# Kernel tuning notes

Hardware: AMD Instinct MI355X
Metric: run time of the kernel (lower is better)

The kernel has to match this reference:

```python
import jax, jax.numpy as jnp
import numpy as np

N = 16384          # replayed items
D_STATE = 2048     # state_dim
D_SEM = 1024       # semantic_dim
S = 4096           # num_semantic_slots
LR = 0.01
DIST_THRESH = 2.0


def setup_inputs() -> dict:
    key = jax.random.key(0)
    k1, k2, k3 = jax.random.split(key, 3)
    replayed_states = jax.random.normal(k1, (N, D_STATE), dtype=jnp.float32)
    replayed_rewards = jax.random.normal(k2, (N,), dtype=jnp.float32)
    # small weight scale so projected content std ~0.05 -> nearest distances
    # straddle the 2.0 threshold and both branches get exercised
    W = jax.random.normal(k3, (D_SEM, D_STATE), dtype=jnp.float32) * (0.05 / np.sqrt(D_STATE))
    b = jnp.zeros((D_SEM,), dtype=jnp.float32)
    semantic_traces = jnp.zeros((S, D_SEM), dtype=jnp.float32)
    trace_strengths = jnp.zeros((S,), dtype=jnp.float32)
    return {
        "replayed_states": replayed_states,
        "replayed_rewards": replayed_rewards,
        "W": W,
        "b": b,
        "semantic_traces": semantic_traces,
        "trace_strengths": trace_strengths,
    }


def _consolidate(content_all, rewards, traces0, strengths0):
    slot_ids = jnp.arange(S, dtype=jnp.int32)

    def step(carry, xs):
        traces, strengths, ptr, num = carry
        content, reward = xs
        reward = jnp.abs(reward)
        valid = jnp.minimum(num, S)
        # euclidean distances to valid slots (invalid -> +inf)
        d = jnp.sqrt(jnp.sum((traces - content[None, :]) ** 2, axis=1))
        d = jnp.where(slot_ids < valid, d, jnp.inf)
        nearest = jnp.argmin(d).astype(jnp.int32)
        nearest_dist = d[nearest]
        do_update = (num > 0) & (nearest_dist < DIST_THRESH)

        # branch A: EMA update of nearest slot
        eff_lr = LR * (1.0 + reward)
        delta = content - traces[nearest]
        traces_u = traces.at[nearest].add(delta * eff_lr)
        strengths_u = strengths.at[nearest].add(1.0)

        # branch B: insert at ring-buffer ptr
        traces_i = traces.at[ptr].set(content)
        strengths_i = strengths.at[ptr].set(1.0)
        ptr_i = (ptr + 1) % S
        num_i = jnp.minimum(num + 1, S)

        traces_n = jnp.where(do_update, traces_u, traces_i)
        strengths_n = jnp.where(do_update, strengths_u, strengths_i)
        ptr_n = jnp.where(do_update, ptr, ptr_i)
        num_n = jnp.where(do_update, num, num_i)
        return (traces_n, strengths_n, ptr_n, num_n), None

    init = (traces0, strengths0, jnp.int32(0), jnp.int32(0))
    (traces, strengths, ptr, num), _ = jax.lax.scan(step, init, (content_all, rewards))
    return traces, strengths, num


def reference(replayed_states, replayed_rewards, W, b, semantic_traces, trace_strengths):
    # projection: nn.Linear -> x @ W.T + b
    content_all = replayed_states @ W.T + b  # (N, D_SEM)
    traces, strengths, num = _consolidate(
        content_all, replayed_rewards, semantic_traces, trace_strengths
    )
    valid_mask = (jnp.arange(S) < jnp.minimum(num, S)).astype(jnp.float32)
    denom = jnp.maximum(valid_mask.sum(), 1.0)
    mean_strength = jnp.where(num > 0, (strengths * valid_mask).sum() / denom, 0.0)
    num_consolidated = jnp.int32(N)  # every item either updates or inserts
    return traces, strengths, num, num_consolidated, mean_strength


if __name__ == "__main__":
    out = reference(**setup_inputs())
    print([getattr(o, "shape", o) for o in out])
```

## Files before the change

### kernel.cpp

```cpp
#include <hip/hip_runtime.h>
#include <cstdint>
#include <cstddef>

#define N_ITEMS 16384
#define D_STATE 2048
#define D_SEM   1024
#define S_SLOTS 4096
#define DTHRESH 2.0f

#define B_ITEMS 256
#define NBLK    (N_ITEMS / B_ITEMS)
#define CHUNK_BLKS 16
#define CHUNK_ITEMS (B_ITEMS * CHUNK_BLKS)

typedef unsigned long long u64;
typedef unsigned int u32;

__global__ __launch_bounds__(256)
void gemm_kernel(const float* __restrict__ A, const float* __restrict__ W,
                 const float* __restrict__ bias, float* __restrict__ C) {
  __shared__ float As[16][68];
  __shared__ float Bs[16][68];
  const int t = threadIdx.x;
  const int ty = t >> 4, tx = t & 15;
  const int i0 = blockIdx.x * 64, j0 = blockIdx.y * 64;
  const int lrow = t >> 2, lcol = (t & 3) << 2;
  float acc[4][4] = {{0.f}};
  const float* ap = A + (size_t)(i0 + lrow) * D_STATE + lcol;
  const float* wp = W + (size_t)(j0 + lrow) * D_STATE + lcol;
  for (int k0 = 0; k0 < D_STATE; k0 += 16) {
    float4 av = *(const float4*)(ap + k0);
    float4 wv = *(const float4*)(wp + k0);
    __syncthreads();
    As[lcol + 0][lrow] = av.x; As[lcol + 1][lrow] = av.y;
    As[lcol + 2][lrow] = av.z; As[lcol + 3][lrow] = av.w;
    Bs[lcol + 0][lrow] = wv.x; Bs[lcol + 1][lrow] = wv.y;
    Bs[lcol + 2][lrow] = wv.z; Bs[lcol + 3][lrow] = wv.w;
    __syncthreads();
#pragma unroll
    for (int kk = 0; kk < 16; kk++) {
      float a[4], b[4];
#pragma unroll
      for (int y = 0; y < 4; y++) a[y] = As[kk][ty * 4 + y];
#pragma unroll
      for (int x = 0; x < 4; x++) b[x] = Bs[kk][tx * 4 + x];
#pragma unroll
      for (int y = 0; y < 4; y++)
#pragma unroll
        for (int x = 0; x < 4; x++) acc[y][x] = fmaf(a[y], b[x], acc[y][x]);
    }
  }
#pragma unroll
  for (int y = 0; y < 4; y++)
#pragma unroll
    for (int x = 0; x < 4; x++) {
      const int col = j0 + tx * 4 + x;
      C[(size_t)(i0 + ty * 4 + y) * D_SEM + col] = acc[y][x] + bias[col];
    }
}

__global__ __launch_bounds__(256)
void gram_kernel(const float* __restrict__ Cc, float* __restrict__ G) {
  const int z = blockIdx.z;
  const float* A = Cc + (size_t)z * B_ITEMS * D_SEM;
  __shared__ float As[16][68];
  __shared__ float Bs[16][68];
  const int t = threadIdx.x;
  const int ty = t >> 4, tx = t & 15;
  const int i0 = blockIdx.x * 64, j0 = blockIdx.y * 64;
  const int lrow = t >> 2, lcol = (t & 3) << 2;
  float acc[4][4] = {{0.f}};
  const float* ap = A + (size_t)(i0 + lrow) * D_SEM + lcol;
  const float* wp = A + (size_t)(j0 + lrow) * D_SEM + lcol;
  for (int k0 = 0; k0 < D_SEM; k0 += 16) {
    float4 av = *(const float4*)(ap + k0);
    float4 wv = *(const float4*)(wp + k0);
    __syncthreads();
    As[lcol + 0][lrow] = av.x; As[lcol + 1][lrow] = av.y;
    As[lcol + 2][lrow] = av.z; As[lcol + 3][lrow] = av.w;
    Bs[lcol + 0][lrow] = wv.x; Bs[lcol + 1][lrow] = wv.y;
    Bs[lcol + 2][lrow] = wv.z; Bs[lcol + 3][lrow] = wv.w;
    __syncthreads();
#pragma unroll
    for (int kk = 0; kk < 16; kk++) {
      float a[4], b[4];
#pragma unroll
      for (int y = 0; y < 4; y++) a[y] = As[kk][ty * 4 + y];
#pragma unroll
      for (int x = 0; x < 4; x++) b[x] = Bs[kk][tx * 4 + x];
#pragma unroll
      for (int y = 0; y < 4; y++)
#pragma unroll
        for (int x = 0; x < 4; x++) acc[y][x] = fmaf(a[y], b[x], acc[y][x]);
    }
  }
  float* Gz = G + (size_t)z * B_ITEMS * B_ITEMS;
#pragma unroll
  for (int y = 0; y < 4; y++)
#pragma unroll
    for (int x = 0; x < 4; x++)
      Gz[(size_t)(i0 + ty * 4 + y) * B_ITEMS + j0 + tx * 4 + x] = acc[y][x];
}

__global__ __launch_bounds__(256)
void pgemm_kernel(const float* __restrict__ A,
                  const float* __restrict__ T,
                  float* __restrict__ P,
                  const int* __restrict__ state) {
  const int limit = min(state[0] + B_ITEMS, S_SLOTS);
  const int j0 = blockIdx.y * 64;
  const int i0 = blockIdx.x * 64;
  const int t = threadIdx.x;
  const int ty = t >> 4, tx = t & 15;
  if (j0 >= limit) {
    const float4 z = {0.f, 0.f, 0.f, 0.f};
    const int col = j0 + tx * 4;
#pragma unroll
    for (int y = 0; y < 4; y++)
      *(float4*)(P + (size_t)(i0 + ty * 4 + y) * S_SLOTS + col) = z;
    return;
  }
  __shared__ float As[16][68];
  __shared__ float Bs[16][68];
  const int lrow = t >> 2, lcol = (t & 3) << 2;
  float acc[4][4] = {{0.f}};
  const float* ap = A + (size_t)(i0 + lrow) * D_SEM + lcol;
  const float* wp = T + (size_t)(j0 + lrow) * D_SEM + lcol;
  for (int k0 = 0; k0 < D_SEM; k0 += 16) {
    float4 av = *(const float4*)(ap + k0);
    float4 wv = *(const float4*)(wp + k0);
    __syncthreads();
    As[lcol + 0][lrow] = av.x; As[lcol + 1][lrow] = av.y;
    As[lcol + 2][lrow] = av.z; As[lcol + 3][lrow] = av.w;
    Bs[lcol + 0][lrow] = wv.x; Bs[lcol + 1][lrow] = wv.y;
    Bs[lcol + 2][lrow] = wv.z; Bs[lcol + 3][lrow] = wv.w;
    __syncthreads();
#pragma unroll
    for (int kk = 0; kk < 16; kk++) {
      float a[4], b[4];
#pragma unroll
      for (int y = 0; y < 4; y++) a[y] = As[kk][ty * 4 + y];
#pragma unroll
      for (int x = 0; x < 4; x++) b[x] = Bs[kk][tx * 4 + x];
#pragma unroll
      for (int y = 0; y < 4; y++)
#pragma unroll
        for (int x = 0; x < 4; x++) acc[y][x] = fmaf(a[y], b[x], acc[y][x]);
    }
  }
#pragma unroll
  for (int y = 0; y < 4; y++)
#pragma unroll
    for (int x = 0; x < 4; x++)
      P[(size_t)(i0 + ty * 4 + y) * S_SLOTS + j0 + tx * 4 + x] = acc[y][x];
}

__global__ __launch_bounds__(256)
void init_kernel(const float* __restrict__ traces0, float* __restrict__ out,
                 float* __restrict__ n_g, int* __restrict__ state) {
  __shared__ float wsum[4];
  const int s = blockIdx.x, t = threadIdx.x;
  const int lane = t & 63, wave = t >> 6;
  float4 v = *(const float4*)(traces0 + (size_t)s * D_SEM + 4 * t);
  *(float4*)(out + (size_t)s * D_SEM + 4 * t) = v;
  float nn = v.x * v.x + v.y * v.y + v.z * v.z + v.w * v.w;
#pragma unroll
  for (int o = 32; o; o >>= 1) nn += __shfl_down(nn, o, 64);
  if (lane == 0) wsum[wave] = nn;
  __syncthreads();
  if (t == 0) n_g[s] = wsum[0] + wsum[1] + wsum[2] + wsum[3];
  if (s == 0 && t == 0) { state[0] = 0; state[1] = 0; }
}

__device__ __forceinline__ float wave_min_f32(float x) {
  int xi = __float_as_int(x), y;
  y = __builtin_amdgcn_update_dpp(xi, xi, 0x111, 0xF, 0xF, false);
  x = fminf(x, __int_as_float(y)); xi = __float_as_int(x);
  y = __builtin_amdgcn_update_dpp(xi, xi, 0x112, 0xF, 0xF, false);
  x = fminf(x, __int_as_float(y)); xi = __float_as_int(x);
  y = __builtin_amdgcn_update_dpp(xi, xi, 0x114, 0xF, 0xF, false);
  x = fminf(x, __int_as_float(y)); xi = __float_as_int(x);
  y = __builtin_amdgcn_update_dpp(xi, xi, 0x118, 0xF, 0xF, false);
  x = fminf(x, __int_as_float(y)); xi = __float_as_int(x);
  y = __builtin_amdgcn_update_dpp(xi, xi, 0x142, 0xA, 0xF, false);
  x = fminf(x, __int_as_float(y)); xi = __float_as_int(x);
  y = __builtin_amdgcn_update_dpp(xi, xi, 0x143, 0xC, 0xF, false);
  x = fminf(x, __int_as_float(y)); xi = __float_as_int(x);
  return __int_as_float(__builtin_amdgcn_readlane(xi, 63));
}

#define CORR_SZ 4352
#define SWZ(s) ((s) + ((s) >> 4))

__global__ __launch_bounds__(512, 1)
void scan_kernel(const float* __restrict__ P, const float* __restrict__ Gb,
                 const float* __restrict__ rewards, const float* __restrict__ n_g,
                 int* __restrict__ state, u64* __restrict__ decs) {
  __shared__ float corr0[CORR_SZ];
  __shared__ float corr1[CORR_SZ];
  __shared__ float grow[8][B_ITEMS];
  __shared__ float rew_l[B_ITEMS];
  __shared__ u64 partials[2][8];
  const int t = threadIdx.x;
  const int lane = t & 63, wave = t >> 6;
  const int s_base = t << 3;
  const int c_base = s_base + (t >> 1);

  int num = state[0];
  int ptr = state[1];

  for (int s = t; s < CORR_SZ; s += 512) { corr0[s] = 0.f; corr1[s] = 0.f; }
  if (t < B_ITEMS) {
    rew_l[t] = rewards[t];
    grow[0][t] = Gb[t];
    grow[1][t] = Gb[B_ITEMS + t];
  }
  float pend_a = (t < B_ITEMS) ? Gb[2 * B_ITEMS + t] : 0.f;
  float pend_b = (t < B_ITEMS) ? Gb[3 * B_ITEMS + t] : 0.f;

  float n_reg[8];
#pragma unroll
  for (int k = 0; k < 8; k += 4) {
    float4 nv = *(const float4*)(n_g + s_base + k);
    n_reg[k + 0] = (s_base + k + 0 < num) ? nv.x : __uint_as_float(0x7F800000u);
    n_reg[k + 1] = (s_base + k + 1 < num) ? nv.y : __uint_as_float(0x7F800000u);
    n_reg[k + 2] = (s_base + k + 2 < num) ? nv.z : __uint_as_float(0x7F800000u);
    n_reg[k + 3] = (s_base + k + 3 < num) ? nv.w : __uint_as_float(0x7F800000u);
  }
  float alpha_r[8];
#pragma unroll
  for (int k = 0; k < 8; k++) alpha_r[k] = 1.f;

  float p_cur[8];
#pragma unroll
  for (int k = 0; k < 8; k += 4) {
    float4 v0 = *(const float4*)(P + s_base + k);
    p_cur[k] = v0.x; p_cur[k + 1] = v0.y; p_cur[k + 2] = v0.z; p_cur[k + 3] = v0.w;
  }

  float raw_a[8], raw_b[8];
  {
    const float* rp = P + (size_t)S_SLOTS + s_base;
#pragma unroll
    for (int k = 0; k < 8; k += 4) {
      float4 v = *(const float4*)(rp + k);
      raw_a[k] = v.x; raw_a[k + 1] = v.y; raw_a[k + 2] = v.z; raw_a[k + 3] = v.w;
    }
#pragma unroll
    for (int k = 0; k < 8; k++) raw_b[k] = 0.f;
  }

  int my_cslot = -1; float my_coeff = 0.f;
  u32 my_slot = 0; float my_lr = 0.f;

  __syncthreads();

#define OWNFIX(K, I) { const float nold = n_reg[K]; \
    if (upd) { \
      n_reg[K] = omr * omr * nold + 2.0f * lr * omr * p_cur[K] + lr * lr * gi_l; \
      alpha_r[K] = __fmul_rn(alpha_r[K], omr); \
      if ((I) + 1 < B_ITEMS) cv[K] = fmaf(omr, cv[K], __fmul_rn(lr, g1)); \
    } else { n_reg[K] = gi_l; alpha_r[K] = 0.f; \
      if ((I) + 1 < B_ITEMS) cv[K] = g1; } }

#define SCAN_STEP(I, CBUF, RAWC, RAWN, PEND) { \
     \
    if (t < B_ITEMS) { \
      if ((I) + 2 < B_ITEMS) grow[((I) + 2) & 7][t] = PEND; \
      if ((I) + 4 < B_ITEMS) PEND = Gb[(size_t)((I) + 4) * B_ITEMS + t]; \
    } \
     \
    if ((I) + 2 < B_ITEMS) { \
      const float* rp = P + (size_t)((I) + 2) * S_SLOTS + s_base; \
      _Pragma("unroll") \
      for (int k = 0; k < 8; k += 4) { \
        float4 v = *(const float4*)(rp + k); \
        RAWN[k] = v.x; RAWN[k + 1] = v.y; RAWN[k + 2] = v.z; RAWN[k + 3] = v.w; \
      } \
    } \
     \
    const float gi_l = grow[(I) & 7][(I)]; \
    const float riv = rew_l[(I)]; \
    float g1 = 0.f; \
    if ((I) + 1 < B_ITEMS) g1 = grow[(I) & 7][(I) + 1]; \
     \
    if ((I) + 1 < B_ITEMS && my_coeff != 0.f) \
      atomicAdd(&CBUF[SWZ(my_cslot)], \
                __fmul_rn(my_coeff, grow[((I) + 1) & 7][t])); \
     \
    float d2[8]; \
    _Pragma("unroll") \
    for (int k = 0; k < 8; k++) { \
      const float v = fmaf(-2.0f, p_cur[k], n_reg[k] + gi_l); \
      d2[k] = (v > 0.f) ? v : 0.f; \
    } \
    float dloc = d2[0]; \
    _Pragma("unroll") \
    for (int k = 1; k < 8; k++) dloc = fminf(dloc, d2[k]); \
    u32 iloc = 0; \
    _Pragma("unroll") \
    for (int k = 7; k >= 1; k--) if (d2[k] == dloc) iloc = (u32)k; \
    const u32 sloc = (u32)s_base + iloc; \
     \
    const float dmin = wave_min_f32(dloc); \
    const u64 bmask = __ballot(dloc == dmin); \
    const int bl = __ffsll((unsigned long long)bmask) - 1; \
    const u32 swave = (u32)__builtin_amdgcn_readlane((int)sloc, bl); \
    if (lane == 0) \
      partials[(I) & 1][wave] = ((u64)__float_as_uint(dmin) << 32) | swave; \
    asm volatile("s_waitcnt lgkmcnt(0)" ::: "memory"); \
    __builtin_amdgcn_s_barrier(); \
    __builtin_amdgcn_sched_barrier(0); \
     \
    u64 bk = partials[(I) & 1][0]; \
    { u64 v = partials[(I) & 1][1]; if (v < bk) bk = v; \
      v = partials[(I) & 1][2]; if (v < bk) bk = v; \
      v = partials[(I) & 1][3]; if (v < bk) bk = v; \
      v = partials[(I) & 1][4]; if (v < bk) bk = v; \
      v = partials[(I) & 1][5]; if (v < bk) bk = v; \
      v = partials[(I) & 1][6]; if (v < bk) bk = v; \
      v = partials[(I) & 1][7]; if (v < bk) bk = v; } \
    float cv[8]; \
    if ((I) + 1 < B_ITEMS) { \
      _Pragma("unroll") \
      for (int k = 0; k < 8; k++) cv[k] = CBUF[c_base + k]; \
    } else { \
      _Pragma("unroll") \
      for (int k = 0; k < 8; k++) cv[k] = 0.f; \
    } \
    const float d2b = __uint_as_float((u32)(bk >> 32)); \
    const int nslot = (int)(u32)bk; \
    const bool upd = (num > 0) && (d2b < 4.0f); \
    const float lr = __fmul_rn(0.01f, __fadd_rn(1.0f, fabsf(riv))); \
    const int slot = upd ? nslot : ptr; \
    const float omr = 1.0f - lr; \
    if (!upd) { num = min(num + 1, S_SLOTS); ptr = (ptr + 1) & (S_SLOTS - 1); } \
    if ((I) == t) { my_slot = (u32)slot | (upd ? 0x80000000u : 0u); my_lr = lr; } \
    if (my_cslot == slot) my_coeff = upd ? __fmul_rn(my_coeff, omr) : 0.f; \
    if ((I) == t) { my_cslot = slot; my_coeff = upd ? lr : 1.f; } \
     \
    if ((slot >> 3) == t) { \
      switch (slot & 7) { \
        case 0:  OWNFIX(0, I) break; case 1:  OWNFIX(1, I) break; \
        case 2:  OWNFIX(2, I) break; case 3:  OWNFIX(3, I) break; \
        case 4:  OWNFIX(4, I) break; case 5:  OWNFIX(5, I) break; \
        case 6:  OWNFIX(6, I) break; default: OWNFIX(7, I) break; \
      } \
    } \
     \
    if ((I) + 1 < B_ITEMS) { \
      _Pragma("unroll") \
      for (int k = 0; k < 8; k++) { \
        p_cur[k] = fmaf(alpha_r[k], RAWC[k], cv[k]); \
        CBUF[c_base + k] = 0.f; \
      } \
    } \
  }

  for (int i = 0; i < B_ITEMS; i += 2) {
    SCAN_STEP(i,     corr0, raw_a, raw_b, pend_a)
    SCAN_STEP(i + 1, corr1, raw_b, raw_a, pend_b)
  }
#undef SCAN_STEP
#undef OWNFIX

  if (t == 0) { state[0] = num; state[1] = ptr; }
  if (t < B_ITEMS)
    decs[t] = ((u64)__float_as_uint(my_lr) << 32) | (u64)my_slot;
}

__global__ __launch_bounds__(256)
void apply_kernel(const float* __restrict__ content,
                  const u64* __restrict__ decs,
                  float* __restrict__ traces,
                  float* __restrict__ n_g) {
  __shared__ u32 aslot[B_ITEMS];
  __shared__ float alr[B_ITEMS];
  __shared__ float betas[B_ITEMS];
  __shared__ int notowner;
  __shared__ float wsum[4];
  const int t = threadIdx.x, j = blockIdx.x;
  const int lane = t & 63, wave = t >> 6;
  const u64 d = decs[t];
  aslot[t] = (u32)(d & 0xFFFFFFFFull);
  alr[t] = __uint_as_float((u32)(d >> 32));
  if (t == 0) notowner = 0;
  __syncthreads();
  const u32 myslot = aslot[j] & 0x7FFFFFFFu;
  if (t > j && (aslot[t] & 0x7FFFFFFFu) == myslot) notowner = 1;
  __syncthreads();
  if (notowner) return;

  float alpha = 1.f, beta = 0.f;
  for (int k = 0; k < B_ITEMS; k++) {
    const u32 a = aslot[k];
    if ((a & 0x7FFFFFFFu) == myslot) {
      const float lr = alr[k];
      if (a & 0x80000000u) {
        const float om = 1.f - lr;
        alpha *= om; beta *= om;
        if (t == k) beta += lr;
      } else {
        alpha = 0.f; beta = (t == k) ? 1.f : 0.f;
      }
    }
  }
  betas[t] = beta;
  __syncthreads();

  float4 v = *(const float4*)(traces + (size_t)myslot * D_SEM + 4 * t);
  v.x *= alpha; v.y *= alpha; v.z *= alpha; v.w *= alpha;
  for (int k = 0; k < B_ITEMS; k++) {
    if ((aslot[k] & 0x7FFFFFFFu) == myslot) {
      const float bk = betas[k];
      const float4 c = *(const float4*)(content + (size_t)k * D_SEM + 4 * t);
      v.x = fmaf(bk, c.x, v.x); v.y = fmaf(bk, c.y, v.y);
      v.z = fmaf(bk, c.z, v.z); v.w = fmaf(bk, c.w, v.w);
    }
  }
  *(float4*)(traces + (size_t)myslot * D_SEM + 4 * t) = v;
  float nn = v.x * v.x + v.y * v.y + v.z * v.z + v.w * v.w;
#pragma unroll
  for (int o = 32; o; o >>= 1) nn += __shfl_down(nn, o, 64);
  if (lane == 0) wsum[wave] = nn;
  __syncthreads();
  if (t == 0) n_g[myslot] = wsum[0] + wsum[1] + wsum[2] + wsum[3];
}

__global__ __launch_bounds__(256)
void finalize_kernel(const float* __restrict__ strengths0,
                     const u64* __restrict__ decs,
                     const int* __restrict__ state, float* __restrict__ out) {
  __shared__ int last_ins[S_SLOTS];
  __shared__ int cnt[S_SLOTS];
  __shared__ float wsum[4];
  const int t = threadIdx.x, lane = t & 63, wave = t >> 6;
  for (int s = t; s < S_SLOTS; s += 256) { last_ins[s] = -1; cnt[s] = 0; }
  __syncthreads();
  for (int k = t; k < N_ITEMS; k += 256) {
    const u32 dd = (u32)(decs[k] & 0xFFFFFFFFull);
    if (!(dd & 0x80000000u)) atomicMax(&last_ins[(int)dd], k);
  }
  __syncthreads();
  for (int k = t; k < N_ITEMS; k += 256) {
    const u32 dd = (u32)(decs[k] & 0xFFFFFFFFull);
    const int slot = (int)(dd & 0x7FFFFFFFu);
    if ((dd & 0x80000000u) && k > last_ins[slot]) atomicAdd(&cnt[slot], 1);
  }
  __syncthreads();
  const int num = state[0];
  float* outs = out + (size_t)S_SLOTS * D_SEM;
  float lsum = 0.f;
  for (int s = t; s < S_SLOTS; s += 256) {
    const float base = (last_ins[s] >= 0) ? 1.f : strengths0[s];
    const float v = base + (float)cnt[s];
    outs[s] = v;
    if (s < num) lsum += v;
  }
#pragma unroll
  for (int o = 32; o; o >>= 1) lsum += __shfl_down(lsum, o, 64);
  if (lane == 0) wsum[wave] = lsum;
  __syncthreads();
  if (t == 0) {
    const float total = wsum[0] + wsum[1] + wsum[2] + wsum[3];
    float denom = (float)num;
    if (denom < 1.f) denom = 1.f;
    outs[S_SLOTS + 0] = (float)num;
    outs[S_SLOTS + 1] = (float)N_ITEMS;
    outs[S_SLOTS + 2] = (num > 0) ? (total / denom) : 0.f;
  }
}

extern "C" void kernel_launch(void* const* d_in, const int* in_sizes, int n_in,
                              void* d_out, int out_size, void* d_ws, size_t ws_size,
                              hipStream_t stream) {
  const float* states  = (const float*)d_in[0];
  const float* rewards = (const float*)d_in[1];
  const float* W       = (const float*)d_in[2];
  const float* bias    = (const float*)d_in[3];
  const float* traces0 = (const float*)d_in[4];
  const float* str0    = (const float*)d_in[5];
  float* out = (float*)d_out;

  char* p = (char*)d_ws;
  float* cbuf = (float*)p;                 p += (size_t)CHUNK_ITEMS * D_SEM * 4;
  float* P    = (float*)p;                 p += (size_t)B_ITEMS * S_SLOTS * 4;
  float* Gb   = (float*)p;                 p += (size_t)CHUNK_BLKS * B_ITEMS * B_ITEMS * 4;
  float* n_g  = (float*)p;                 p += (size_t)S_SLOTS * 4;
  u64*   decs = (u64*)p;                   p += (size_t)N_ITEMS * 8;
  int*   state = (int*)p;

  init_kernel<<<S_SLOTS, 256, 0, stream>>>(traces0, out, n_g, state);

  for (int c = 0; c < N_ITEMS / CHUNK_ITEMS; c++) {
    gemm_kernel<<<dim3(CHUNK_ITEMS / 64, D_SEM / 64), 256, 0, stream>>>(
        states + (size_t)c * CHUNK_ITEMS * D_STATE, W, bias, cbuf);
    gram_kernel<<<dim3(4, 4, CHUNK_BLKS), 256, 0, stream>>>(cbuf, Gb);
    for (int bb = 0; bb < CHUNK_BLKS; bb++) {
      const int b = c * CHUNK_BLKS + bb;
      const float* cblk = cbuf + (size_t)bb * B_ITEMS * D_SEM;
      const float* Gblk = Gb + (size_t)bb * B_ITEMS * B_ITEMS;
      pgemm_kernel<<<dim3(4, S_SLOTS / 64), 256, 0, stream>>>(cblk, out, P, state);
      scan_kernel<<<1, 512, 0, stream>>>(P, Gblk, rewards + (size_t)b * B_ITEMS,
                                         n_g, state, decs + (size_t)b * B_ITEMS);
      apply_kernel<<<B_ITEMS, 256, 0, stream>>>(cblk, decs + (size_t)b * B_ITEMS,
                                                out, n_g);
    }
  }
  finalize_kernel<<<1, 256, 0, stream>>>(str0, decs, state, out);
}
```

Measured before the change: 29.50 ms.

## Widen sequential scan kernel to 1024 threads with four slots per thread

The single-block scan kernel now runs 1024 threads, each owning 4 slots instead of 8, with 16 waves. This halves the per-thread distance, min and update work on the serial critical path of each scan step. In exchange the cross-wave partial reduction grows from 8 to 16 entries, done as a tree, and each barrier now synchronises twice as many waves.

```diff
diff --git a/kernel.cpp b/kernel.cpp
--- a/kernel.cpp
+++ b/kernel.cpp
@@ -191,8 +191,9 @@
 
 #define CORR_SZ 4352
 #define SWZ(s) ((s) + ((s) >> 4))
-
-__global__ __launch_bounds__(512, 1)
+#define NW 16
+
+__global__ __launch_bounds__(1024, 1)
 void scan_kernel(const float* __restrict__ P, const float* __restrict__ Gb,
                  const float* __restrict__ rewards, const float* __restrict__ n_g,
                  int* __restrict__ state, u64* __restrict__ decs) {
@@ -200,16 +201,16 @@
   __shared__ float corr1[CORR_SZ];
   __shared__ float grow[8][B_ITEMS];
   __shared__ float rew_l[B_ITEMS];
-  __shared__ u64 partials[2][8];
+  __shared__ u64 partials[2][NW];
   const int t = threadIdx.x;
   const int lane = t & 63, wave = t >> 6;
-  const int s_base = t << 3;
-  const int c_base = s_base + (t >> 1);
+  const int s_base = t << 2;
+  const int c_base = s_base + (t >> 2);
 
   int num = state[0];
   int ptr = state[1];
 
-  for (int s = t; s < CORR_SZ; s += 512) { corr0[s] = 0.f; corr1[s] = 0.f; }
+  for (int s = t; s < CORR_SZ; s += 1024) { corr0[s] = 0.f; corr1[s] = 0.f; }
   if (t < B_ITEMS) {
     rew_l[t] = rewards[t];
     grow[0][t] = Gb[t];
@@ -218,36 +219,30 @@
   float pend_a = (t < B_ITEMS) ? Gb[2 * B_ITEMS + t] : 0.f;
   float pend_b = (t < B_ITEMS) ? Gb[3 * B_ITEMS + t] : 0.f;
 
-  float n_reg[8];
-#pragma unroll
-  for (int k = 0; k < 8; k += 4) {
-    float4 nv = *(const float4*)(n_g + s_base + k);
-    n_reg[k + 0] = (s_base + k + 0 < num) ? nv.x : __uint_as_float(0x7F800000u);
-    n_reg[k + 1] = (s_base + k + 1 < num) ? nv.y : __uint_as_float(0x7F800000u);
-    n_reg[k + 2] = (s_base + k + 2 < num) ? nv.z : __uint_as_float(0x7F800000u);
-    n_reg[k + 3] = (s_base + k + 3 < num) ? nv.w : __uint_as_float(0x7F800000u);
-  }
-  float alpha_r[8];
-#pragma unroll
-  for (int k = 0; k < 8; k++) alpha_r[k] = 1.f;
-
-  float p_cur[8];
-#pragma unroll
-  for (int k = 0; k < 8; k += 4) {
-    float4 v0 = *(const float4*)(P + s_base + k);
-    p_cur[k] = v0.x; p_cur[k + 1] = v0.y; p_cur[k + 2] = v0.z; p_cur[k + 3] = v0.w;
-  }
-
-  float raw_a[8], raw_b[8];
+  float n_reg[4];
   {
-    const float* rp = P + (size_t)S_SLOTS + s_base;
-#pragma unroll
-    for (int k = 0; k < 8; k += 4) {
-      float4 v = *(const float4*)(rp + k);
-      raw_a[k] = v.x; raw_a[k + 1] = v.y; raw_a[k + 2] = v.z; raw_a[k + 3] = v.w;
-    }
-#pragma unroll
-    for (int k = 0; k < 8; k++) raw_b[k] = 0.f;
+    float4 nv = *(const float4*)(n_g + s_base);
+    n_reg[0] = (s_base + 0 < num) ? nv.x : __uint_as_float(0x7F800000u);
+    n_reg[1] = (s_base + 1 < num) ? nv.y : __uint_as_float(0x7F800000u);
+    n_reg[2] = (s_base + 2 < num) ? nv.z : __uint_as_float(0x7F800000u);
+    n_reg[3] = (s_base + 3 < num) ? nv.w : __uint_as_float(0x7F800000u);
+  }
+  float alpha_r[4];
+#pragma unroll
+  for (int k = 0; k < 4; k++) alpha_r[k] = 1.f;
+
+  float p_cur[4];
+  {
+    float4 v0 = *(const float4*)(P + s_base);
+    p_cur[0] = v0.x; p_cur[1] = v0.y; p_cur[2] = v0.z; p_cur[3] = v0.w;
+  }
+
+  float raw_a[4], raw_b[4];
+  {
+    float4 v = *(const float4*)(P + (size_t)S_SLOTS + s_base);
+    raw_a[0] = v.x; raw_a[1] = v.y; raw_a[2] = v.z; raw_a[3] = v.w;
+#pragma unroll
+    for (int k = 0; k < 4; k++) raw_b[k] = 0.f;
   }
 
   int my_cslot = -1; float my_coeff = 0.f;
@@ -271,12 +266,8 @@
     } \
      \
     if ((I) + 2 < B_ITEMS) { \
-      const float* rp = P + (size_t)((I) + 2) * S_SLOTS + s_base; \
-      _Pragma("unroll") \
-      for (int k = 0; k < 8; k += 4) { \
-        float4 v = *(const float4*)(rp + k); \
-        RAWN[k] = v.x; RAWN[k + 1] = v.y; RAWN[k + 2] = v.z; RAWN[k + 3] = v.w; \
-      } \
+      float4 v = *(const float4*)(P + (size_t)((I) + 2) * S_SLOTS + s_base); \
+      RAWN[0] = v.x; RAWN[1] = v.y; RAWN[2] = v.z; RAWN[3] = v.w; \
     } \
      \
     const float gi_l = grow[(I) & 7][(I)]; \
@@ -288,18 +279,18 @@
       atomicAdd(&CBUF[SWZ(my_cslot)], \
                 __fmul_rn(my_coeff, grow[((I) + 1) & 7][t])); \
      \
-    float d2[8]; \
+    float d2[4]; \
     _Pragma("unroll") \
-    for (int k = 0; k < 8; k++) { \
+    for (int k = 0; k < 4; k++) { \
       const float v = fmaf(-2.0f, p_cur[k], n_reg[k] + gi_l); \
       d2[k] = (v > 0.f) ? v : 0.f; \
     } \
-    float dloc = d2[0]; \
-    _Pragma("unroll") \
-    for (int k = 1; k < 8; k++) dloc = fminf(dloc, d2[k]); \
+    float dloc = fminf(fminf(d2[0], d2[1]), fminf(d2[2], d2[3])); \
     u32 iloc = 0; \
-    _Pragma("unroll") \
-    for (int k = 7; k >= 1; k--) if (d2[k] == dloc) iloc = (u32)k; \
+    if (d2[3] == dloc) iloc = 3u; \
+    if (d2[2] == dloc) iloc = 2u; \
+    if (d2[1] == dloc) iloc = 1u; \
+    if (d2[0] == dloc) iloc = 0u; \
     const u32 sloc = (u32)s_base + iloc; \
      \
     const float dmin = wave_min_f32(dloc); \
@@ -312,21 +303,22 @@
     __builtin_amdgcn_s_barrier(); \
     __builtin_amdgcn_sched_barrier(0); \
      \
-    u64 bk = partials[(I) & 1][0]; \
-    { u64 v = partials[(I) & 1][1]; if (v < bk) bk = v; \
-      v = partials[(I) & 1][2]; if (v < bk) bk = v; \
-      v = partials[(I) & 1][3]; if (v < bk) bk = v; \
-      v = partials[(I) & 1][4]; if (v < bk) bk = v; \
-      v = partials[(I) & 1][5]; if (v < bk) bk = v; \
-      v = partials[(I) & 1][6]; if (v < bk) bk = v; \
-      v = partials[(I) & 1][7]; if (v < bk) bk = v; } \
-    float cv[8]; \
+    u64 pv[NW]; \
+    _Pragma("unroll") \
+    for (int k = 0; k < NW; k++) pv[k] = partials[(I) & 1][k]; \
+    _Pragma("unroll") \
+    for (int st = 1; st < NW; st <<= 1) \
+      _Pragma("unroll") \
+      for (int k = 0; k < NW; k += 2 * st) \
+        if (pv[k + st] < pv[k]) pv[k] = pv[k + st]; \
+    const u64 bk = pv[0]; \
+    float cv[4]; \
     if ((I) + 1 < B_ITEMS) { \
       _Pragma("unroll") \
-      for (int k = 0; k < 8; k++) cv[k] = CBUF[c_base + k]; \
+      for (int k = 0; k < 4; k++) cv[k] = CBUF[c_base + k]; \
     } else { \
       _Pragma("unroll") \
-      for (int k = 0; k < 8; k++) cv[k] = 0.f; \
+      for (int k = 0; k < 4; k++) cv[k] = 0.f; \
     } \
     const float d2b = __uint_as_float((u32)(bk >> 32)); \
     const int nslot = (int)(u32)bk; \
@@ -339,18 +331,16 @@
     if (my_cslot == slot) my_coeff = upd ? __fmul_rn(my_coeff, omr) : 0.f; \
     if ((I) == t) { my_cslot = slot; my_coeff = upd ? lr : 1.f; } \
      \
-    if ((slot >> 3) == t) { \
-      switch (slot & 7) { \
+    if ((slot >> 2) == t) { \
+      switch (slot & 3) { \
         case 0:  OWNFIX(0, I) break; case 1:  OWNFIX(1, I) break; \
-        case 2:  OWNFIX(2, I) break; case 3:  OWNFIX(3, I) break; \
-        case 4:  OWNFIX(4, I) break; case 5:  OWNFIX(5, I) break; \
-        case 6:  OWNFIX(6, I) break; default: OWNFIX(7, I) break; \
+        case 2:  OWNFIX(2, I) break; default: OWNFIX(3, I) break; \
       } \
     } \
      \
     if ((I) + 1 < B_ITEMS) { \
       _Pragma("unroll") \
-      for (int k = 0; k < 8; k++) { \
+      for (int k = 0; k < 4; k++) { \
         p_cur[k] = fmaf(alpha_r[k], RAWC[k], cv[k]); \
         CBUF[c_base + k] = 0.f; \
       } \
@@ -501,8 +491,8 @@
       const float* cblk = cbuf + (size_t)bb * B_ITEMS * D_SEM;
       const float* Gblk = Gb + (size_t)bb * B_ITEMS * B_ITEMS;
       pgemm_kernel<<<dim3(4, S_SLOTS / 64), 256, 0, stream>>>(cblk, out, P, state);
-      scan_kernel<<<1, 512, 0, stream>>>(P, Gblk, rewards + (size_t)b * B_ITEMS,
-                                         n_g, state, decs + (size_t)b * B_ITEMS);
+      scan_kernel<<<1, 1024, 0, stream>>>(P, Gblk, rewards + (size_t)b * B_ITEMS,
+                                          n_g, state, decs + (size_t)b * B_ITEMS);
       apply_kernel<<<B_ITEMS, 256, 0, stream>>>(cblk, decs + (size_t)b * B_ITEMS,
                                                 out, n_g);
     }
```

Measured after the change: 35.92 ms. 21.8% more time.
